# Performance work log

Hardware: AMD Instinct MI355X
Metric: run time of the kernel (lower is better)

Reference implementation:

```python
import jax, jax.numpy as jnp
import numpy as np

FEAT_STRIDE = 16
SCALES = np.array([8.0, 16.0, 32.0])
RATIOS = np.array([0.5, 1.0, 2.0])
A = 9  # anchors per location
PRE_NMS_TOPN = 6000   # TEST config (module in eval mode)
POST_NMS_TOPN = 300
NMS_THRESH = 0.7


def _generate_anchors(base_size=16):
    base = np.array([1.0, 1.0, base_size, base_size]) - 1.0  # [0,0,15,15]
    w = base[2] - base[0] + 1.0
    h = base[3] - base[1] + 1.0
    xc = base[0] + 0.5 * (w - 1.0)
    yc = base[1] + 0.5 * (h - 1.0)
    size = w * h
    ws = np.round(np.sqrt(size / RATIOS))
    hs = np.round(ws * RATIOS)
    ratio_anchors = np.stack([xc - 0.5 * (ws - 1), yc - 0.5 * (hs - 1),
                              xc + 0.5 * (ws - 1), yc + 0.5 * (hs - 1)], axis=1)
    out = []
    for ra in ratio_anchors:
        rw = ra[2] - ra[0] + 1.0
        rh = ra[3] - ra[1] + 1.0
        rxc = ra[0] + 0.5 * (rw - 1.0)
        ryc = ra[1] + 0.5 * (rh - 1.0)
        sw = rw * SCALES
        sh = rh * SCALES
        out.append(np.stack([rxc - 0.5 * (sw - 1), ryc - 0.5 * (sh - 1),
                             rxc + 0.5 * (sw - 1), ryc + 0.5 * (sh - 1)], axis=1))
    return np.concatenate(out, 0).astype(np.float32)  # [9,4]


def _all_anchors(H, W):
    a = _generate_anchors()
    sx = np.arange(W) * float(FEAT_STRIDE)
    sy = np.arange(H) * float(FEAT_STRIDE)
    sx, sy = np.meshgrid(sx, sy)
    shifts = np.stack([sx.ravel(), sy.ravel(), sx.ravel(), sy.ravel()], 1)  # [H*W,4]
    return (shifts[:, None, :] + a[None, :, :]).reshape(-1, 4).astype(np.float32)  # [H*W*A,4]


def _nms_sorted(boxes):
    # boxes: [N,4] already sorted by descending score; greedy NMS -> [POST_NMS_TOPN,4]
    x1, y1, x2, y2 = boxes[:, 0], boxes[:, 1], boxes[:, 2], boxes[:, 3]
    areas = (x2 - x1 + 1.0) * (y2 - y1 + 1.0)

    def body(i, st):
        valid, out_b = st
        idx = jnp.argmax(valid)          # first still-valid (highest score) box
        has = valid[idx]
        b = boxes[idx]
        xx1 = jnp.maximum(b[0], x1)
        yy1 = jnp.maximum(b[1], y1)
        xx2 = jnp.minimum(b[2], x2)
        yy2 = jnp.minimum(b[3], y2)
        inter = jnp.maximum(xx2 - xx1 + 1.0, 0.0) * jnp.maximum(yy2 - yy1 + 1.0, 0.0)
        iou = inter / (areas[idx] + areas - inter)
        valid = valid & (iou <= NMS_THRESH)  # suppresses idx itself (iou=1)
        out_b = out_b.at[i].set(jnp.where(has, b, jnp.zeros_like(b)))
        return valid, out_b

    valid0 = jnp.ones(boxes.shape[0], bool)
    out0 = jnp.zeros((POST_NMS_TOPN, 4), boxes.dtype)
    _, out_b = jax.lax.fori_loop(0, POST_NMS_TOPN, body, (valid0, out0))
    return out_b


def _rpn_forward(base_feat, im_info, W_conv, b_conv, W_cls, b_cls, W_bbox, b_bbox):
    B, C, H, W = base_feat.shape
    rpn_conv = jax.nn.relu(
        jax.lax.conv_general_dilated(base_feat, W_conv, (1, 1), 'SAME',
                                     dimension_numbers=('NCHW', 'OIHW', 'NCHW'))
        + b_conv[None, :, None, None])
    # 1x1 heads as channel matmuls
    cls_score = jnp.einsum('bchw,oc->bohw', rpn_conv, W_cls) + b_cls[None, :, None, None]
    bbox_pred = jnp.einsum('bchw,oc->bohw', rpn_conv, W_bbox) + b_bbox[None, :, None, None]
    # reshape(x,2) + softmax(dim=1) + reshape back == softmax over the (bg,fg) pair per anchor
    prob = jax.nn.softmax(cls_score.reshape(B, 2, A, H, W), axis=1)
    fg_scores = prob[:, 1].transpose(0, 2, 3, 1).reshape(B, -1)        # [B, H*W*A]
    deltas = bbox_pred.transpose(0, 2, 3, 1).reshape(B, -1, 4)         # [B, H*W*A, 4]

    anchors = jnp.asarray(_all_anchors(H, W))                          # [N,4]
    aw = anchors[:, 2] - anchors[:, 0] + 1.0
    ah = anchors[:, 3] - anchors[:, 1] + 1.0
    acx = anchors[:, 0] + 0.5 * aw
    acy = anchors[:, 1] + 0.5 * ah
    pcx = deltas[..., 0] * aw + acx
    pcy = deltas[..., 1] * ah + acy
    pw = jnp.exp(deltas[..., 2]) * aw
    ph = jnp.exp(deltas[..., 3]) * ah
    proposals = jnp.stack([pcx - 0.5 * pw, pcy - 0.5 * ph,
                           pcx + 0.5 * pw, pcy + 0.5 * ph], axis=-1)   # [B,N,4]
    imh = im_info[:, 0][:, None]
    imw = im_info[:, 1][:, None]
    proposals = jnp.stack([jnp.clip(proposals[..., 0], 0.0, imw - 1.0),
                           jnp.clip(proposals[..., 1], 0.0, imh - 1.0),
                           jnp.clip(proposals[..., 2], 0.0, imw - 1.0),
                           jnp.clip(proposals[..., 3], 0.0, imh - 1.0)], axis=-1)

    _, top_idx = jax.lax.top_k(fg_scores, PRE_NMS_TOPN)                # pre-NMS top-k
    top_boxes = jnp.take_along_axis(proposals, top_idx[..., None], axis=1)  # [B,K,4]
    kept = jax.vmap(_nms_sorted)(top_boxes)                            # [B,POST,4]
    batch_idx = jnp.broadcast_to(
        jnp.arange(B, dtype=kept.dtype)[:, None, None], (B, POST_NMS_TOPN, 1))
    rois = jnp.concatenate([batch_idx, kept], axis=-1)                 # [B,POST,5]
    return rois


def setup_inputs() -> dict:
    key = jax.random.key(0)
    ks = jax.random.split(key, 5)
    B, C, H, W = 4, 512, 64, 64
    base_feat = jax.random.normal(ks[0], (B, C, H, W), jnp.float32)
    im_info = jnp.tile(jnp.array([H * 16.0, W * 16.0, 1.0], jnp.float32), (B, 1))
    gt_boxes = jnp.zeros((B, 20, 5), jnp.float32)
    num_boxes = jnp.zeros((B,), jnp.int32)
    W_conv = jax.random.normal(ks[1], (512, C, 3, 3), jnp.float32) * 0.01
    b_conv = jnp.zeros((512,), jnp.float32)
    W_cls = jax.random.normal(ks[2], (2 * A, 512), jnp.float32) * 0.01
    b_cls = jnp.zeros((2 * A,), jnp.float32)
    W_bbox = jax.random.normal(ks[3], (4 * A, 512), jnp.float32) * 0.01
    b_bbox = jnp.zeros((4 * A,), jnp.float32)
    return {"base_feat": base_feat, "im_info": im_info, "gt_boxes": gt_boxes,
            "num_boxes": num_boxes, "W_conv": W_conv, "b_conv": b_conv,
            "W_cls": W_cls, "b_cls": b_cls, "W_bbox": W_bbox, "b_bbox": b_bbox}


def reference(base_feat, im_info, gt_boxes, num_boxes, W_conv, b_conv, W_cls, b_cls, W_bbox, b_bbox):
    # Eval-mode RPN: rois from ProposalLayer; rpn losses are 0 in eval.
    rois = _rpn_forward(base_feat, im_info, W_conv, b_conv, W_cls, b_cls, W_bbox, b_bbox)
    return rois
```

## Files before the change

### kernel.cpp

```cpp
#include <hip/hip_runtime.h>
#include <math.h>

constexpr int NB = 4;
constexpr int NC = 512;
constexpr int NH = 64, NW = 64;
constexpr int NPOS = NH * NW;
constexpr int NANCH = NPOS * 9;
constexpr int PRE_TOPN = 6000;
constexpr int POST_TOPN = 300;
constexpr int CAND_CAP = 40960;

typedef short short8_t __attribute__((ext_vector_type(8)));
typedef float f32x4_t __attribute__((ext_vector_type(4)));

__device__ __constant__ float A9c[9][4] = {
  {-84.f,-40.f,99.f,55.f},   {-176.f,-88.f,191.f,103.f}, {-360.f,-184.f,375.f,199.f},
  {-56.f,-56.f,71.f,71.f},   {-120.f,-120.f,135.f,135.f},{-248.f,-248.f,263.f,263.f},
  {-36.f,-80.f,51.f,95.f},   {-80.f,-168.f,95.f,183.f},  {-168.f,-344.f,183.f,359.f}};

constexpr size_t OFF_WB   = 0;
constexpr size_t OFF_IT   = 14155776;
constexpr size_t OFF_CONV = 47710208;
constexpr size_t OFF_HIST = 81264640;
constexpr size_t OFF_MISC = 81330176;
constexpr size_t OFF_HEAD = 0;
constexpr size_t OFF_SKEY = 3538944;
constexpr size_t OFF_BOX  = 4128768;
constexpr size_t OFF_CKEY = 6488064;
constexpr size_t OFF_CIDX = 7143424;
constexpr size_t OFF_SBOX = 7798784;

__device__ inline unsigned short f2bf(float f) {
  unsigned u = __float_as_uint(f);
  unsigned r = u + 0x7fffu + ((u >> 16) & 1u);
  return (unsigned short)(r >> 16);
}
__device__ inline float bf2f(unsigned short h) { return __uint_as_float(((unsigned)h) << 16); }

__device__ inline void split8(const float4 A, const float4 B, short8_t& h, short8_t& m, short8_t& l) {
#define SPL(J, X) { unsigned short hh = f2bf(X); float fh = bf2f(hh); \
                    unsigned short mm = f2bf((X) - fh); float fm = bf2f(mm); \
                    unsigned short ll = f2bf((X) - fh - fm); \
                    h[J] = (short)hh; m[J] = (short)mm; l[J] = (short)ll; }
  SPL(0, A.x) SPL(1, A.y) SPL(2, A.z) SPL(3, A.w)
  SPL(4, B.x) SPL(5, B.y) SPL(6, B.z) SPL(7, B.w)
#undef SPL
}

__global__ __launch_bounds__(256) void wsplit_k(const float* __restrict__ Wc,
                                               short* __restrict__ Wb) {
  const int i = blockIdx.x * 256 + threadIdx.x;
  const int tap = i >> 18;
  const int ko = (i >> 9) & 511, c = i & 511;
  const float w = Wc[(size_t)ko * 4608 + c * 9 + tap];
  const unsigned short h = f2bf(w);
  const float fh = bf2f(h);
  const unsigned short m = f2bf(w - fh);
  const float fm = bf2f(m);
  const unsigned short l = f2bf(w - fh - fm);
  const size_t base = ((size_t)tap * 3 * 512 + ko) * 512 + c;
  Wb[base] = (short)h;
  Wb[base + 512 * 512] = (short)m;
  Wb[base + 2 * 512 * 512] = (short)l;
}

__global__ __launch_bounds__(256) void cvtI_k(const float* __restrict__ in,
                                              float* __restrict__ It) {
  __shared__ float T[64][65];
  const int b = blockIdx.z, c0 = blockIdx.y * 64, pos0 = blockIdx.x * 64;
  const int tid = threadIdx.x;
  for (int i = tid; i < 4096; i += 256) {
    int cc = i >> 6, pp = i & 63;
    T[cc][pp] = in[(((size_t)b * 512 + c0 + cc) << 12) + pos0 + pp];
  }
  __syncthreads();
  for (int i = tid; i < 4096; i += 256) {
    int pp = i >> 6, cc = i & 63;
    It[((((size_t)b << 12) + pos0 + pp) << 9) + c0 + cc] = T[cc][pp];
  }
}

__global__ __launch_bounds__(256, 2) void conv_mfma_k(
    const float* __restrict__ It, const short* __restrict__ Wb,
    const float* __restrict__ bias, float* __restrict__ out) {
  __shared__ short Slds[3 * 264 * 32];
  __shared__ short Wl[3 * 128 * 32];
  const int tid = threadIdx.x;
  const int wave = tid >> 6, lane = tid & 63;
  const int lm = lane & 15, lg = lane >> 4;
  const int pos0 = blockIdx.x * 128;
  const int ko0  = blockIdx.y * 128;
  const int b    = blockIdx.z;
  const int y0   = pos0 >> 6;

  f32x4_t acc[2][8];
  #pragma unroll
  for (int f = 0; f < 2; ++f)
    #pragma unroll
    for (int p = 0; p < 8; ++p) acc[f][p] = (f32x4_t){0.f, 0.f, 0.f, 0.f};

  short8_t pf[2][3];
#define PREF(TAP, C0S)                                                          \
  { _Pragma("unroll")                                                           \
    for (int t_ = 0; t_ < 2; ++t_) {                                            \
      const int i_ = tid + t_ * 256;                                            \
      const int kol_ = i_ >> 2, part_ = i_ & 3;                                 \
      const size_t g_ = (((size_t)(TAP) * 3) * 512 + ko0 + kol_) * 512 + (C0S) + (part_ << 3); \
      pf[t_][0] = *(const short8_t*)(Wb + g_);                                  \
      pf[t_][1] = *(const short8_t*)(Wb + g_ + 262144);                         \
      pf[t_][2] = *(const short8_t*)(Wb + g_ + 524288);                         \
    } }

  PREF(0, 0)

  for (int c0 = 0; c0 < 512; c0 += 32) {
    __syncthreads();
    for (int i = tid; i < 264; i += 256) {
      int r = i / 66, xx = i - r * 66;
      int gy = y0 + r - 1, gx = xx - 1;
      bool ok = ((unsigned)gy < 64u) && ((unsigned)gx < 64u);
      float4 f0 = {}, f1 = {}, f2 = {}, f3 = {}, f4 = {}, f5 = {}, f6 = {}, f7 = {};
      if (ok) {
        const float4* gp = (const float4*)(It + ((((size_t)b << 12) + (gy << 6) + gx) << 9) + c0);
        f0 = gp[0]; f1 = gp[1]; f2 = gp[2]; f3 = gp[3];
        f4 = gp[4]; f5 = gp[5]; f6 = gp[6]; f7 = gp[7];
      }
      const int sw = (xx >> 1) & 3;
      char* drow = (char*)Slds + (i << 6);
      short8_t h, m, l;
      split8(f0, f1, h, m, l);
      *(short8_t*)(drow + ((0 ^ sw) << 4)) = h;
      *(short8_t*)(drow + 16896 + ((0 ^ sw) << 4)) = m;
      *(short8_t*)(drow + 33792 + ((0 ^ sw) << 4)) = l;
      split8(f2, f3, h, m, l);
      *(short8_t*)(drow + ((1 ^ sw) << 4)) = h;
      *(short8_t*)(drow + 16896 + ((1 ^ sw) << 4)) = m;
      *(short8_t*)(drow + 33792 + ((1 ^ sw) << 4)) = l;
      split8(f4, f5, h, m, l);
      *(short8_t*)(drow + ((2 ^ sw) << 4)) = h;
      *(short8_t*)(drow + 16896 + ((2 ^ sw) << 4)) = m;
      *(short8_t*)(drow + 33792 + ((2 ^ sw) << 4)) = l;
      split8(f6, f7, h, m, l);
      *(short8_t*)(drow + ((3 ^ sw) << 4)) = h;
      *(short8_t*)(drow + 16896 + ((3 ^ sw) << 4)) = m;
      *(short8_t*)(drow + 33792 + ((3 ^ sw) << 4)) = l;
    }
    for (int tap = 0; tap < 9; ++tap) {
      __syncthreads();
      #pragma unroll
      for (int t_ = 0; t_ < 2; ++t_) {
        const int i_ = tid + t_ * 256;
        const int kol_ = i_ >> 2, part_ = i_ & 3;
        char* base = (char*)Wl + (kol_ << 6) + ((part_ ^ ((kol_ >> 1) & 3)) << 4);
        *(short8_t*)(base) = pf[t_][0];
        *(short8_t*)(base + 8192) = pf[t_][1];
        *(short8_t*)(base + 16384) = pf[t_][2];
      }
      __syncthreads();
      {
        const int ntap = (tap == 8) ? 0 : tap + 1;
        const int nc0  = (tap == 8) ? ((c0 + 32 < 512) ? c0 + 32 : c0) : c0;
        PREF(ntap, nc0)
      }
      const int dy = tap / 3, dx = tap - dy * 3;
      short8_t Ah[2], Am[2], Al[2];
      #pragma unroll
      for (int f = 0; f < 2; ++f) {
        int kol = (wave << 5) + (f << 4) + lm;
        char* ab = (char*)Wl + (kol << 6) + ((lg ^ ((kol >> 1) & 3)) << 4);
        Ah[f] = *(short8_t*)ab;
        Am[f] = *(short8_t*)(ab + 8192);
        Al[f] = *(short8_t*)(ab + 16384);
      }
      #pragma unroll
      for (int p = 0; p < 8; ++p) {
        const int yl = p >> 2;
        const int x  = ((p & 3) << 4) + lm;
        const int r  = yl + dy, xx = x + dx;
        char* bb = (char*)Slds + ((r * 66 + xx) << 6) + ((lg ^ ((xx >> 1) & 3)) << 4);
        short8_t Bh = *(short8_t*)bb;
        short8_t Bm = *(short8_t*)(bb + 16896);
        short8_t Bl = *(short8_t*)(bb + 33792);
        #pragma unroll
        for (int f = 0; f < 2; ++f) {
          acc[f][p] = __builtin_amdgcn_mfma_f32_16x16x32_bf16(Ah[f], Bh, acc[f][p], 0, 0, 0);
          acc[f][p] = __builtin_amdgcn_mfma_f32_16x16x32_bf16(Ah[f], Bm, acc[f][p], 0, 0, 0);
          acc[f][p] = __builtin_amdgcn_mfma_f32_16x16x32_bf16(Am[f], Bh, acc[f][p], 0, 0, 0);
          acc[f][p] = __builtin_amdgcn_mfma_f32_16x16x32_bf16(Ah[f], Bl, acc[f][p], 0, 0, 0);
          acc[f][p] = __builtin_amdgcn_mfma_f32_16x16x32_bf16(Al[f], Bh, acc[f][p], 0, 0, 0);
          acc[f][p] = __builtin_amdgcn_mfma_f32_16x16x32_bf16(Am[f], Bm, acc[f][p], 0, 0, 0);
        }
      }
    }
  }
#undef PREF
  #pragma unroll
  for (int f = 0; f < 2; ++f) {
    const int koB = ko0 + (wave << 5) + (f << 4) + (lg << 2);
    #pragma unroll
    for (int reg = 0; reg < 4; ++reg) {
      const float bv = bias[koB + reg];
      #pragma unroll
      for (int p = 0; p < 8; ++p) {
        const int pos = pos0 + (p << 4) + lm;
        out[(((size_t)b * 512 + koB + reg) << 12) + pos] = fmaxf(acc[f][p][reg] + bv, 0.f);
      }
    }
  }
}

__global__ __launch_bounds__(256, 4) void head_mfma_k(
    const float* __restrict__ conv, const float* __restrict__ Wcls,
    const float* __restrict__ bcls, const float* __restrict__ Wbbox,
    const float* __restrict__ bbbox, float* __restrict__ head) {
  __shared__ short Bl[3 * 64 * 32];
  __shared__ short Al[3 * 64 * 32];
  const int tid = threadIdx.x;
  const int wave = tid >> 6, lane = tid & 63;
  const int lm = lane & 15, lg = lane >> 4;
  const int pos0 = blockIdx.x * 64;
  const int b    = blockIdx.y;

  f32x4_t acc[4];
  #pragma unroll
  for (int f = 0; f < 4; ++f) acc[f] = (f32x4_t){0.f, 0.f, 0.f, 0.f};

  const float* cb = conv + ((size_t)b * 512 << 12);

  for (int c0 = 0; c0 < 512; c0 += 32) {
    __syncthreads();
    {
      const int pos_l = tid & 63, ch = tid >> 6;
      float v[8];
      #pragma unroll
      for (int j = 0; j < 8; ++j)
        v[j] = cb[((size_t)(c0 + ch * 8 + j) << 12) + pos0 + pos_l];
      short8_t h, m, l;
      split8(make_float4(v[0], v[1], v[2], v[3]), make_float4(v[4], v[5], v[6], v[7]), h, m, l);
      char* base = (char*)Bl + (pos_l << 6) + ((ch ^ ((pos_l >> 1) & 3)) << 4);
      *(short8_t*)(base) = h;
      *(short8_t*)(base + 4096) = m;
      *(short8_t*)(base + 8192) = l;
    }
    {
      const int ko = tid >> 2, part = tid & 3;
      float4 wa = {}, wb = {};
      if (ko < 54) {
        const float* src = (ko < 18) ? (Wcls + (size_t)ko * 512) : (Wbbox + (size_t)(ko - 18) * 512);
        wa = *(const float4*)(src + c0 + part * 8);
        wb = *(const float4*)(src + c0 + part * 8 + 4);
      }
      short8_t h, m, l;
      split8(wa, wb, h, m, l);
      char* base = (char*)Al + (ko << 6) + ((part ^ ((ko >> 1) & 3)) << 4);
      *(short8_t*)(base) = h;
      *(short8_t*)(base + 4096) = m;
      *(short8_t*)(base + 8192) = l;
    }
    __syncthreads();
    short8_t Bh, Bm, Bv;
    {
      const int pos_l = (wave << 4) + lm;
      char* bb = (char*)Bl + (pos_l << 6) + ((lg ^ ((pos_l >> 1) & 3)) << 4);
      Bh = *(short8_t*)bb;
      Bm = *(short8_t*)(bb + 4096);
      Bv = *(short8_t*)(bb + 8192);
    }
    #pragma unroll
    for (int f = 0; f < 4; ++f) {
      const int kol = (f << 4) + lm;
      char* ab = (char*)Al + (kol << 6) + ((lg ^ ((kol >> 1) & 3)) << 4);
      short8_t Ah = *(short8_t*)ab;
      short8_t Am = *(short8_t*)(ab + 4096);
      short8_t Av = *(short8_t*)(ab + 8192);
      acc[f] = __builtin_amdgcn_mfma_f32_16x16x32_bf16(Ah, Bh, acc[f], 0, 0, 0);
      acc[f] = __builtin_amdgcn_mfma_f32_16x16x32_bf16(Ah, Bm, acc[f], 0, 0, 0);
      acc[f] = __builtin_amdgcn_mfma_f32_16x16x32_bf16(Am, Bh, acc[f], 0, 0, 0);
      acc[f] = __builtin_amdgcn_mfma_f32_16x16x32_bf16(Ah, Bv, acc[f], 0, 0, 0);
      acc[f] = __builtin_amdgcn_mfma_f32_16x16x32_bf16(Av, Bh, acc[f], 0, 0, 0);
      acc[f] = __builtin_amdgcn_mfma_f32_16x16x32_bf16(Am, Bm, acc[f], 0, 0, 0);
    }
  }
  #pragma unroll
  for (int f = 0; f < 4; ++f) {
    #pragma unroll
    for (int reg = 0; reg < 4; ++reg) {
      const int ko = (f << 4) + (lg << 2) + reg;
      if (ko < 54) {
        const float bv = (ko < 18) ? bcls[ko] : bbbox[ko - 18];
        const int pos = pos0 + (wave << 4) + lm;
        head[(((size_t)b * 54 + ko) << 12) + pos] = acc[f][reg] + bv;
      }
    }
  }
}

__global__ __launch_bounds__(256) void decode_k(
    const float* __restrict__ head, const float* __restrict__ im_info,
    float* __restrict__ boxes, unsigned* __restrict__ skeys, unsigned* __restrict__ hist) {
  __shared__ unsigned hl[4096];
  const int tid = threadIdx.x;
  #pragma unroll
  for (int i = 0; i < 16; ++i) hl[tid + i * 256] = 0u;
  __syncthreads();
  const int p = blockIdx.x * 256 + tid;
  const int b = p >> 12; const int pos = p & 4095;
  const int x = pos & 63; const int y = pos >> 6;
  const float* hb = head + ((size_t)b * 54 << 12);
  const float imh = im_info[b * 3 + 0], imw = im_info[b * 3 + 1];
  float s[18];
  #pragma unroll
  for (int o = 0; o < 18; ++o) s[o] = hb[(o << 12) + pos];
  float d[36];
  #pragma unroll
  for (int o = 0; o < 36; ++o) d[o] = hb[((18 + o) << 12) + pos];
  const float sx = x * 16.f, sy = y * 16.f;
  #pragma unroll
  for (int a = 0; a < 9; ++a) {
    const float s0 = s[a], s1 = s[9 + a];
    const float m = fmaxf(s0, s1);
    const float e0 = expf(s0 - m), e1 = expf(s1 - m);
    const float score = e1 / (e0 + e1);
    const float d0 = d[a * 4 + 0], d1 = d[a * 4 + 1];
    const float d2 = d[a * 4 + 2], d3 = d[a * 4 + 3];
    const float ax1 = A9c[a][0] + sx, ay1 = A9c[a][1] + sy;
    const float ax2 = A9c[a][2] + sx, ay2 = A9c[a][3] + sy;
    const float aw = ax2 - ax1 + 1.f, ah = ay2 - ay1 + 1.f;
    const float acx = ax1 + 0.5f * aw, acy = ay1 + 0.5f * ah;
    const float pcx = d0 * aw + acx, pcy = d1 * ah + acy;
    const float pw = expf(d2) * aw, ph = expf(d3) * ah;
    const float x1 = fminf(fmaxf(pcx - 0.5f * pw, 0.f), imw - 1.f);
    const float y1 = fminf(fmaxf(pcy - 0.5f * ph, 0.f), imh - 1.f);
    const float x2 = fminf(fmaxf(pcx + 0.5f * pw, 0.f), imw - 1.f);
    const float y2 = fminf(fmaxf(pcy + 0.5f * ph, 0.f), imh - 1.f);
    const int n = pos * 9 + a;
    *(float4*)&boxes[((size_t)b * NANCH + n) * 4] = make_float4(x1, y1, x2, y2);
    const unsigned key = __float_as_uint(score);
    skeys[(size_t)b * NANCH + n] = key;
    atomicAdd(&hl[key >> 20], 1u);
  }
  __syncthreads();
  #pragma unroll
  for (int i = 0; i < 16; ++i) {
    unsigned c = hl[tid + i * 256];
    if (c) atomicAdd(&hist[b * 4096 + tid + i * 256], c);
  }
}

__global__ __launch_bounds__(512) void select_k(
    const unsigned* __restrict__ skeys, const unsigned* __restrict__ hist,
    unsigned* __restrict__ misc, unsigned* __restrict__ ckey,
    unsigned* __restrict__ cidx) {
  const int b = blockIdx.x;
  const int tid = threadIdx.x;
  __shared__ unsigned csum[256];
  __shared__ unsigned hl2[256];
  __shared__ unsigned s_t1, s_cumAbove, s_T2, s_cnt;
  const unsigned* h = hist + b * 4096;
  if (tid < 256) {
    unsigned s = 0;
    #pragma unroll
    for (int i = 0; i < 16; ++i) s += h[tid * 16 + i];
    csum[tid] = s;
    hl2[tid] = 0u;
  }
  __syncthreads();
  if (tid == 0) {
    unsigned cum = 0; int chunk = 0;
    for (int c = 255; c >= 0; --c) {
      if (cum + csum[c] >= (unsigned)PRE_TOPN) { chunk = c; break; }
      cum += csum[c];
    }
    unsigned t1 = chunk * 16, cumAbove = cum;
    for (int i = 15; i >= 0; --i) {
      unsigned cnt = h[chunk * 16 + i];
      if (cum + cnt >= (unsigned)PRE_TOPN) { t1 = chunk * 16 + i; cumAbove = cum; break; }
      cum += cnt;
    }
    s_t1 = t1; s_cumAbove = cumAbove; s_cnt = 0u;
  }
  __syncthreads();
  const unsigned t1 = s_t1;
  const unsigned* sk = skeys + (size_t)b * NANCH;
  for (int t = tid; t < NANCH; t += 512) {
    unsigned key = sk[t];
    if ((key >> 20) == t1) atomicAdd(&hl2[(key >> 12) & 255u], 1u);
  }
  __syncthreads();
  if (tid == 0) {
    unsigned cum = s_cumAbove;
    unsigned T2 = t1 << 20;
    for (int ss = 255; ss >= 0; --ss) {
      unsigned c = hl2[ss];
      if (cum + c >= (unsigned)PRE_TOPN) { T2 = (t1 << 20) | ((unsigned)ss << 12); break; }
      cum += c;
    }
    s_T2 = T2;
  }
  __syncthreads();
  const unsigned T2 = s_T2;
  const int lane = tid & 63;
  for (int t = tid; t < NANCH; t += 512) {
    unsigned key = sk[t];
    bool pred = key >= T2;
    unsigned long long mb = __ballot(pred);
    unsigned base = 0;
    if (lane == 0) base = atomicAdd(&s_cnt, (unsigned)__popcll(mb));
    base = (unsigned)__shfl((int)base, 0, 64);
    if (pred) {
      unsigned pp = base + (unsigned)__popcll(mb & ((1ull << lane) - 1ull));
      if (pp < (unsigned)CAND_CAP) {
        ckey[(size_t)b * CAND_CAP + pp] = key;
        cidx[(size_t)b * CAND_CAP + pp] = (unsigned)t;
      }
    }
  }
  __syncthreads();
  if (tid == 0) misc[12 + b] = s_cnt;
}

__global__ __launch_bounds__(256) void rank_scatter_k(
    const unsigned* __restrict__ ckey, const unsigned* __restrict__ cidx,
    const unsigned* __restrict__ misc, const float* __restrict__ boxes,
    float* __restrict__ sbox) {
  const int b = blockIdx.y;
  const int K = min((int)misc[12 + b], CAND_CAP);
  const int i = blockIdx.x * 256 + threadIdx.x;
  unsigned mykey = 0, myidx = 0;
  const bool active = i < K;
  if (active) {
    mykey = ckey[(size_t)b * CAND_CAP + i];
    myidx = cidx[(size_t)b * CAND_CAP + i];
  }
  int rank = 0;
  __shared__ unsigned skey[1024];
  __shared__ unsigned sidx[1024];
  for (int c0 = 0; c0 < K; c0 += 1024) {
    int n = min(1024, K - c0);
    __syncthreads();
    for (int e = threadIdx.x; e < n; e += 256) {
      skey[e] = ckey[(size_t)b * CAND_CAP + c0 + e];
      sidx[e] = cidx[(size_t)b * CAND_CAP + c0 + e];
    }
    __syncthreads();
    if (active) {
      for (int j = 0; j < n; ++j) {
        unsigned kj = skey[j];
        rank += (kj > mykey) || (kj == mykey && sidx[j] < myidx);
      }
    }
  }
  if (active && rank < PRE_TOPN) {
    float4 bx = *(const float4*)&boxes[((size_t)b * NANCH + myidx) * 4];
    *(float4*)&sbox[((size_t)b * PRE_TOPN + rank) * 4] = bx;
  }
}

__global__ __launch_bounds__(256) void nms_fused_k(const float* __restrict__ sbox,
                                                   float* __restrict__ out) {
  __shared__ float4 tb[64];
  __shared__ float4 pk[POST_TOPN];
  __shared__ unsigned long long supw[4];
  __shared__ int s_np;
  const int b = blockIdx.x;
  const int tid = threadIdx.x;
  const int wv = tid >> 6, lane = tid & 63;
  const float* S = sbox + (size_t)b * PRE_TOPN * 4;
  float* O = out + (size_t)b * POST_TOPN * 5;
  if (tid == 0) s_np = 0;
  int np = 0;

  for (int t = 0; t < (PRE_TOPN + 63) / 64; ++t) {
    __syncthreads();
    np = s_np;
    if (np >= POST_TOPN) break;
    const int nt = min(64, PRE_TOPN - t * 64);
    if (tid < 64 && tid < nt) tb[tid] = *(const float4*)&S[(size_t)(t * 64 + tid) * 4];
    __syncthreads();
    const float4 q = tb[lane < nt ? lane : 0];
    const float qarea = (q.z - q.x + 1.f) * (q.w - q.y + 1.f);
    bool sup = false;
    for (int p = wv; p < np; p += 4) {
      const float4 pb = pk[p];
      const float pa = (pb.z - pb.x + 1.f) * (pb.w - pb.y + 1.f);
      const float xx1 = fmaxf(pb.x, q.x), yy1 = fmaxf(pb.y, q.y);
      const float xx2 = fminf(pb.z, q.z), yy2 = fminf(pb.w, q.w);
      const float inter = fmaxf(xx2 - xx1 + 1.f, 0.f) * fmaxf(yy2 - yy1 + 1.f, 0.f);
      const float iou = inter / (pa + qarea - inter);
      sup = sup || (iou > 0.7f);
    }
    unsigned long long bal = __ballot(sup);
    if (lane == 0) supw[wv] = bal;
    __syncthreads();
    if (wv == 0) {
      const unsigned long long validm = (nt == 64) ? ~0ull : ((1ull << nt) - 1ull);
      unsigned long long remaining = validm & ~(supw[0] | supw[1] | supw[2] | supw[3]);
      while (remaining && np < POST_TOPN) {
        const int jj = __ffsll((long long)remaining) - 1;
        const float4 pb = tb[jj];
        if (lane == 0) {
          pk[np] = pb;
          O[np * 5 + 0] = (float)b;
          O[np * 5 + 1] = pb.x; O[np * 5 + 2] = pb.y;
          O[np * 5 + 3] = pb.z; O[np * 5 + 4] = pb.w;
        }
        const float pa = (pb.z - pb.x + 1.f) * (pb.w - pb.y + 1.f);
        const float xx1 = fmaxf(pb.x, q.x), yy1 = fmaxf(pb.y, q.y);
        const float xx2 = fminf(pb.z, q.z), yy2 = fminf(pb.w, q.w);
        const float inter = fmaxf(xx2 - xx1 + 1.f, 0.f) * fmaxf(yy2 - yy1 + 1.f, 0.f);
        const float iou = inter / (pa + qarea - inter);
        remaining &= ~__ballot(iou > 0.7f);
        ++np;
      }
      if (lane == 0) s_np = np;
    }
  }
  __syncthreads();
  np = s_np;
  for (int e = tid; e < (POST_TOPN - np) * 5; e += 256) {
    int r = np + e / 5; int c = e - (e / 5) * 5;
    O[r * 5 + c] = (c == 0) ? (float)b : 0.f;
  }
}

extern "C" void kernel_launch(void* const* d_in, const int* in_sizes, int n_in,
                              void* d_out, int out_size, void* d_ws, size_t ws_size,
                              hipStream_t stream) {
  const float* base_feat = (const float*)d_in[0];
  const float* im_info   = (const float*)d_in[1];
  const float* W_conv    = (const float*)d_in[4];
  const float* b_conv    = (const float*)d_in[5];
  const float* W_cls     = (const float*)d_in[6];
  const float* b_cls     = (const float*)d_in[7];
  const float* W_bbox    = (const float*)d_in[8];
  const float* b_bbox    = (const float*)d_in[9];
  float* out = (float*)d_out;
  char* ws = (char*)d_ws;

  short*    Wb    = (short*)(ws + OFF_WB);
  float*    It    = (float*)(ws + OFF_IT);
  float*    conv  = (float*)(ws + OFF_CONV);
  float*    head  = (float*)(ws + OFF_HEAD);
  unsigned* skeys = (unsigned*)(ws + OFF_SKEY);
  float*    boxes = (float*)(ws + OFF_BOX);
  unsigned* hist  = (unsigned*)(ws + OFF_HIST);
  unsigned* misc  = (unsigned*)(ws + OFF_MISC);
  unsigned* ckey  = (unsigned*)(ws + OFF_CKEY);
  unsigned* cidx  = (unsigned*)(ws + OFF_CIDX);
  float*    sbox  = (float*)(ws + OFF_SBOX);

  hipMemsetAsync(ws + OFF_HIST, 0, 65536 + 256, stream);

  wsplit_k<<<9216, 256, 0, stream>>>(W_conv, Wb);
  cvtI_k<<<dim3(64, 8, 4), 256, 0, stream>>>(base_feat, It);
  conv_mfma_k<<<dim3(32, 4, 4), 256, 0, stream>>>(It, Wb, b_conv, conv);
  head_mfma_k<<<dim3(64, 4), 256, 0, stream>>>(conv, W_cls, b_cls, W_bbox, b_bbox, head);
  decode_k<<<64, 256, 0, stream>>>(head, im_info, boxes, skeys, hist);
  select_k<<<4, 512, 0, stream>>>(skeys, hist, misc, ckey, cidx);
  rank_scatter_k<<<dim3(CAND_CAP / 256, 4), 256, 0, stream>>>(ckey, cidx, misc, boxes, sbox);
  nms_fused_k<<<4, 256, 0, stream>>>(sbox, out);
}
```

Baseline: 733.6 us.

## Precompute bf16 triple split of input in transpose kernel instead of conv loop

The transpose kernel now writes the input as three bf16 planes (high, mid, low) in NHWC layout, so the conv kernel only copies pre-split shorts into shared memory. Before, every conv block recomputed the split for each halo tile, and each tile is reused by four output-channel blocks and across neighbouring rows. In exchange the conv kernel reads 1.5x more bytes from global memory, since three 16-bit planes replace one fp32 plane. Separately, rank_scatter blocks whose range lies beyond the candidate count now exit early.

Result: no change. 741.0 us (+1.0%).

```diff
diff --git a/kernel.cpp b/kernel.cpp
--- a/kernel.cpp
+++ b/kernel.cpp
@@ -13,16 +13,18 @@
 typedef short short8_t __attribute__((ext_vector_type(8)));
 typedef float f32x4_t __attribute__((ext_vector_type(4)));
 
+constexpr size_t IPLANE = (size_t)NB * NPOS * 512;
+
 __device__ __constant__ float A9c[9][4] = {
   {-84.f,-40.f,99.f,55.f},   {-176.f,-88.f,191.f,103.f}, {-360.f,-184.f,375.f,199.f},
   {-56.f,-56.f,71.f,71.f},   {-120.f,-120.f,135.f,135.f},{-248.f,-248.f,263.f,263.f},
   {-36.f,-80.f,51.f,95.f},   {-80.f,-168.f,95.f,183.f},  {-168.f,-344.f,183.f,359.f}};
 
 constexpr size_t OFF_WB   = 0;
-constexpr size_t OFF_IT   = 14155776;
-constexpr size_t OFF_CONV = 47710208;
-constexpr size_t OFF_HIST = 81264640;
-constexpr size_t OFF_MISC = 81330176;
+constexpr size_t OFF_IB   = 14155776;
+constexpr size_t OFF_CONV = 64487424;
+constexpr size_t OFF_HIST = 98041856;
+constexpr size_t OFF_MISC = 98107392;
 constexpr size_t OFF_HEAD = 0;
 constexpr size_t OFF_SKEY = 3538944;
 constexpr size_t OFF_BOX  = 4128768;
@@ -64,8 +66,8 @@
   Wb[base + 2 * 512 * 512] = (short)l;
 }
 
-__global__ __launch_bounds__(256) void cvtI_k(const float* __restrict__ in,
-                                              float* __restrict__ It) {
+__global__ __launch_bounds__(256) void cvt_split_k(const float* __restrict__ in,
+                                                   short* __restrict__ Ib) {
   __shared__ float T[64][65];
   const int b = blockIdx.z, c0 = blockIdx.y * 64, pos0 = blockIdx.x * 64;
   const int tid = threadIdx.x;
@@ -74,14 +76,24 @@
     T[cc][pp] = in[(((size_t)b * 512 + c0 + cc) << 12) + pos0 + pp];
   }
   __syncthreads();
-  for (int i = tid; i < 4096; i += 256) {
-    int pp = i >> 6, cc = i & 63;
-    It[((((size_t)b << 12) + pos0 + pp) << 9) + c0 + cc] = T[cc][pp];
+  #pragma unroll
+  for (int it = 0; it < 2; ++it) {
+    const int i = it * 256 + tid;
+    const int pp = i >> 3, cpart = i & 7;
+    float v[8];
+    #pragma unroll
+    for (int j = 0; j < 8; ++j) v[j] = T[cpart * 8 + j][pp];
+    short8_t h, m, l;
+    split8(make_float4(v[0], v[1], v[2], v[3]), make_float4(v[4], v[5], v[6], v[7]), h, m, l);
+    const size_t dst = ((((size_t)b << 12) + pos0 + pp) << 9) + c0 + (cpart << 3);
+    *(short8_t*)(Ib + dst) = h;
+    *(short8_t*)(Ib + IPLANE + dst) = m;
+    *(short8_t*)(Ib + 2 * IPLANE + dst) = l;
   }
 }
 
 __global__ __launch_bounds__(256, 2) void conv_mfma_k(
-    const float* __restrict__ It, const short* __restrict__ Wb,
+    const short* __restrict__ Ib, const short* __restrict__ Wb,
     const float* __restrict__ bias, float* __restrict__ out) {
   __shared__ short Slds[3 * 264 * 32];
   __shared__ short Wl[3 * 128 * 32];
@@ -116,34 +128,21 @@
   for (int c0 = 0; c0 < 512; c0 += 32) {
     __syncthreads();
     for (int i = tid; i < 264; i += 256) {
-      int r = i / 66, xx = i - r * 66;
-      int gy = y0 + r - 1, gx = xx - 1;
-      bool ok = ((unsigned)gy < 64u) && ((unsigned)gx < 64u);
-      float4 f0 = {}, f1 = {}, f2 = {}, f3 = {}, f4 = {}, f5 = {}, f6 = {}, f7 = {};
-      if (ok) {
-        const float4* gp = (const float4*)(It + ((((size_t)b << 12) + (gy << 6) + gx) << 9) + c0);
-        f0 = gp[0]; f1 = gp[1]; f2 = gp[2]; f3 = gp[3];
-        f4 = gp[4]; f5 = gp[5]; f6 = gp[6]; f7 = gp[7];
-      }
+      const int r = i / 66, xx = i - r * 66;
+      const int gy = y0 + r - 1, gx = xx - 1;
+      const bool ok = ((unsigned)gy < 64u) && ((unsigned)gx < 64u);
+      const size_t src = ((((size_t)b << 12) + (gy << 6) + gx) << 9) + c0;
       const int sw = (xx >> 1) & 3;
       char* drow = (char*)Slds + (i << 6);
-      short8_t h, m, l;
-      split8(f0, f1, h, m, l);
-      *(short8_t*)(drow + ((0 ^ sw) << 4)) = h;
-      *(short8_t*)(drow + 16896 + ((0 ^ sw) << 4)) = m;
-      *(short8_t*)(drow + 33792 + ((0 ^ sw) << 4)) = l;
-      split8(f2, f3, h, m, l);
-      *(short8_t*)(drow + ((1 ^ sw) << 4)) = h;
-      *(short8_t*)(drow + 16896 + ((1 ^ sw) << 4)) = m;
-      *(short8_t*)(drow + 33792 + ((1 ^ sw) << 4)) = l;
-      split8(f4, f5, h, m, l);
-      *(short8_t*)(drow + ((2 ^ sw) << 4)) = h;
-      *(short8_t*)(drow + 16896 + ((2 ^ sw) << 4)) = m;
-      *(short8_t*)(drow + 33792 + ((2 ^ sw) << 4)) = l;
-      split8(f6, f7, h, m, l);
-      *(short8_t*)(drow + ((3 ^ sw) << 4)) = h;
-      *(short8_t*)(drow + 16896 + ((3 ^ sw) << 4)) = m;
-      *(short8_t*)(drow + 33792 + ((3 ^ sw) << 4)) = l;
+      #pragma unroll
+      for (int pl = 0; pl < 3; ++pl) {
+        #pragma unroll
+        for (int part = 0; part < 4; ++part) {
+          short8_t v = {};
+          if (ok) v = *(const short8_t*)(Ib + (size_t)pl * IPLANE + src + (part << 3));
+          *(short8_t*)(drow + pl * 16896 + ((part ^ sw) << 4)) = v;
+        }
+      }
     }
     for (int tap = 0; tap < 9; ++tap) {
       __syncthreads();
@@ -425,6 +424,7 @@
     float* __restrict__ sbox) {
   const int b = blockIdx.y;
   const int K = min((int)misc[12 + b], CAND_CAP);
+  if (blockIdx.x * 256 >= (unsigned)K) return;
   const int i = blockIdx.x * 256 + threadIdx.x;
   unsigned mykey = 0, myidx = 0;
   const bool active = i < K;
@@ -538,7 +538,7 @@
   char* ws = (char*)d_ws;
 
   short*    Wb    = (short*)(ws + OFF_WB);
-  float*    It    = (float*)(ws + OFF_IT);
+  short*    Ib    = (short*)(ws + OFF_IB);
   float*    conv  = (float*)(ws + OFF_CONV);
   float*    head  = (float*)(ws + OFF_HEAD);
   unsigned* skeys = (unsigned*)(ws + OFF_SKEY);
@@ -552,8 +552,8 @@
   hipMemsetAsync(ws + OFF_HIST, 0, 65536 + 256, stream);
 
   wsplit_k<<<9216, 256, 0, stream>>>(W_conv, Wb);
-  cvtI_k<<<dim3(64, 8, 4), 256, 0, stream>>>(base_feat, It);
-  conv_mfma_k<<<dim3(32, 4, 4), 256, 0, stream>>>(It, Wb, b_conv, conv);
+  cvt_split_k<<<dim3(64, 8, 4), 256, 0, stream>>>(base_feat, Ib);
+  conv_mfma_k<<<dim3(32, 4, 4), 256, 0, stream>>>(Ib, Wb, b_conv, conv);
   head_mfma_k<<<dim3(64, 4), 256, 0, stream>>>(conv, W_cls, b_cls, W_bbox, b_bbox, head);
   decode_k<<<64, 256, 0, stream>>>(head, im_info, boxes, skeys, hist);
   select_k<<<4, 512, 0, stream>>>(skeys, hist, misc, ckey, cidx);
```
